# Kernel optimization log

Measured on AMD Instinct MI355X. Metric: run time of the kernel, lower is better.

Reference implementation:

```python
import jax, jax.numpy as jnp
import numpy as np

NUM_HEADS = 8
D_MODEL = 512
HEAD_DIM = D_MODEL // NUM_HEADS


def _conv1x1(x, W, b):
    # Conv1d(kernel_size=1): x [B, Cin, N], W [Cout, Cin], b [Cout] -> [B, Cout, N]
    return jnp.einsum('oi,bin->bon', W, x) + b[None, :, None]


def setup_inputs() -> dict:
    key = jax.random.key(0)
    ks = jax.random.split(key, 12)
    B, D, N, Mlen = 4, D_MODEL, 2048, 2048
    inp = {
        'query': jax.random.normal(ks[0], (B, D, N), dtype=jnp.float32),
        'key':   jax.random.normal(ks[1], (B, D, Mlen), dtype=jnp.float32),
        'value': jax.random.normal(ks[2], (B, D, Mlen), dtype=jnp.float32),
        'M':     jnp.ones((B, N, Mlen), dtype=jnp.int32),
    }
    scale = 0.02
    inp['Wq'] = jax.random.normal(ks[3], (D, D), dtype=jnp.float32) * scale
    inp['bq'] = jnp.zeros((D,), dtype=jnp.float32)
    inp['Wk'] = jax.random.normal(ks[4], (D, D), dtype=jnp.float32) * scale
    inp['bk'] = jnp.zeros((D,), dtype=jnp.float32)
    inp['Wv'] = jax.random.normal(ks[5], (D, D), dtype=jnp.float32) * scale
    inp['bv'] = jnp.zeros((D,), dtype=jnp.float32)
    inp['Wm'] = jax.random.normal(ks[6], (D, D), dtype=jnp.float32) * scale
    inp['bm'] = jnp.zeros((D,), dtype=jnp.float32)
    return inp


def reference(query, key, value, M, Wq, bq, Wk, bk, Wv, bv, Wm, bm):
    B = query.shape[0]
    # 1x1-conv projections, then channel split as [head_dim, heads] (matches torch .view)
    q = _conv1x1(query, Wq, bq).reshape(B, HEAD_DIM, NUM_HEADS, -1)  # [B, d, h, N]
    k = _conv1x1(key,   Wk, bk).reshape(B, HEAD_DIM, NUM_HEADS, -1)  # [B, d, h, M]
    v = _conv1x1(value, Wv, bv).reshape(B, HEAD_DIM, NUM_HEADS, -1)  # [B, d, h, M]
    scores = jnp.einsum('bdhn,bdhm->bhnm', q, k) / jnp.sqrt(jnp.float32(HEAD_DIM))
    # mask: positions with M==0 are disallowed -> fill with -finfo.max
    bad = (1 - M)[:, None, :, :].astype(bool)  # [B, 1, N, M], broadcasts over heads
    scores = jnp.where(bad, -jnp.finfo(scores.dtype).max, scores)
    prob = jax.nn.softmax(scores, axis=-1)  # [B, h, N, M]
    x = jnp.einsum('bhnm,bdhm->bdhn', prob, v)  # [B, d, h, N]
    out = _conv1x1(x.reshape(B, HEAD_DIM * NUM_HEADS, -1), Wm, bm)  # [B, D, N]
    return out
```

## Files before the change

### kernel.cpp

```cpp
#include <hip/hip_runtime.h>

typedef __attribute__((ext_vector_type(8))) short s8v;
typedef __attribute__((ext_vector_type(4))) float f4v;
typedef _Float16 h4 __attribute__((ext_vector_type(4)));
typedef unsigned short u16;
typedef unsigned long long u64;

#define DM 512
#define NH 8
#define HD 64
#define BB 4
#define NN 2048

__device__ __forceinline__ float bf2f(u16 x){ return __uint_as_float(((unsigned)x)<<16); }
__device__ __forceinline__ u16 f2bf(float f){
  unsigned u = __float_as_uint(f);
  u += 0x7FFFu + ((u>>16)&1u);
  return (u16)(u>>16);
}
__device__ __forceinline__ void gl2lds16(const u16* g, u16* l){
  __builtin_amdgcn_global_load_lds((__attribute__((address_space(1))) void*)(g),
                                   (__attribute__((address_space(3))) void*)(l), 16, 0, 0);
}

__global__ void k_permute(const float* Wq, const float* bq, const float* Wk, const float* bk,
                          const float* Wv, const float* bv, const float* Wm,
                          u16* Wp, u16* Wmp, float* bp){
  int blk = blockIdx.x, tid = threadIdx.x;
  if (blk < 1536){
    int t = blk >> 9, op = blk & 511;
    int srow = ((op & 63) << 3) | (op >> 6);
    const float* W = (t==0) ? Wq : ((t==1) ? Wk : Wv);
    for (int j = tid; j < 512; j += 256)
      Wp[((size_t)t*512 + op)*512 + j] = f2bf(W[(size_t)srow*512 + j]);
  } else if (blk < 2048){
    int o = blk - 1536;
    for (int c = tid; c < 512; c += 256){
      int scol = ((c & 63) << 3) | (c >> 6);
      Wmp[(size_t)o*512 + c] = f2bf(Wm[(size_t)o*512 + scol]);
    }
  } else {
    for (int idx = tid; idx < 1536; idx += 256){
      int t = idx >> 9, op = idx & 511;
      const float* bs = (t==0) ? bq : ((t==1) ? bk : bv);
      int srow = ((op & 63) << 3) | (op >> 6);
      bp[idx] = bs[srow];
    }
  }
}

__global__ __launch_bounds__(256) void k_transpose(const float* q, const float* k, const float* v, u16* XT){
  __shared__ u16 T[64*72];
  int blk = blockIdx.x, tid = threadIdx.x;
  int rt = blk & 31; blk >>= 5;
  int it = blk & 7;  blk >>= 3;
  int b  = blk & 3;  int t = blk >> 2;
  const float* src = (t==0) ? q : ((t==1) ? k : v);
  src += (size_t)b*DM*NN;
  int i0 = it*64, r0 = rt*64;
  int il = tid>>4, rj = (tid&15)*4;
  #pragma unroll
  for (int p=0;p<4;p++){
    int i = il + p*16;
    float4 vv = *(const float4*)&src[(size_t)(i0+i)*NN + r0 + rj];
    float fv[4] = {vv.x, vv.y, vv.z, vv.w};
    #pragma unroll
    for (int qq=0;qq<4;qq++){
      int r = rj + qq;
      int sr = ((r&3)<<4) | (r>>2);
      T[sr*72 + i] = f2bf(fv[qq]);
    }
  }
  __syncthreads();
  u16* dst = XT + ((size_t)(t*4+b)*NN)*DM;
  int rl = tid>>3, ib = (tid&7)*8;
  #pragma unroll
  for (int p=0;p<2;p++){
    int r = rl + p*32;
    int sr = ((r&3)<<4) | (r>>2);
    s8v vv = *(s8v*)&T[sr*72 + ib];
    *(s8v*)&dst[(size_t)(r0+r)*DM + i0 + ib] = vv;
  }
}

__global__ __launch_bounds__(256) void k_proj(const u16* XT, const u16* Wp, const float* bp,
                                              u16* P, u16* VT){
  __shared__ u16 Al[128*32];
  __shared__ u16 Bl[128*32];
  __shared__ u16 S[128*72];
  int blk = blockIdx.x, tid = threadIdx.x;
  int nt = blk & 3; int mt = blk >> 2;
  int tb = mt >> 4;
  int t  = tb >> 2, b = tb & 3;
  int r0 = (mt & 15)*128, o0 = nt*128;
  const u16* Abase = XT + ((size_t)tb*NN + r0)*DM;
  const u16* Bbase = Wp + ((size_t)t*512 + o0)*DM;

  int w = tid>>6, L = tid&63, li = L&15, lq = L>>4;
  int wr = w>>1, wc = w&1;
  int srow = tid>>2;
  int g8   = ((tid&3) ^ ((tid>>3)&3))*8;
  u16* AldsW = &Al[((tid&192))*8];
  u16* BldsW = &Bl[((tid&192))*8];
  int sw = (li>>1)&3;

  f4v acc[4][4];
  #pragma unroll
  for (int a=0;a<4;a++)
    #pragma unroll
    for (int c2=0;c2<4;c2++) acc[a][c2] = (f4v){0.f,0.f,0.f,0.f};

  for (int kk=0; kk<16; kk++){
    int k0 = kk*32;
    __syncthreads();
    #pragma unroll
    for (int c=0;c<2;c++){
      gl2lds16(&Abase[(size_t)(srow + c*64)*DM + k0 + g8], AldsW + c*2048);
      gl2lds16(&Bbase[(size_t)(srow + c*64)*DM + k0 + g8], BldsW + c*2048);
    }
    __syncthreads();
    s8v af[4], bfr[4];
    #pragma unroll
    for (int a=0;a<4;a++){
      int r = wr*64 + a*16 + li;
      af[a] = *(s8v*)&Al[r*32 + ((lq ^ sw))*8];
    }
    #pragma unroll
    for (int c2=0;c2<4;c2++){
      int r = wc*64 + c2*16 + li;
      bfr[c2] = *(s8v*)&Bl[r*32 + ((lq ^ sw))*8];
    }
    #pragma unroll
    for (int a=0;a<4;a++)
      #pragma unroll
      for (int c2=0;c2<4;c2++)
        acc[a][c2] = __builtin_amdgcn_mfma_f32_16x16x32_bf16(af[a], bfr[c2], acc[a][c2], 0, 0, 0);
  }

  if (t < 2){
    float scale = (t==0) ? 0.125f : 1.0f;
    #pragma unroll
    for (int c2=0;c2<4;c2++){
      int col = wc*64 + c2*16 + li;
      int h = (o0 + col) >> 6, d = col & 63;
      float bias = bp[t*512 + o0 + col];
      u16* Pb = P + (((size_t)tb*NH + h)*NN)*HD + d;
      #pragma unroll
      for (int a=0;a<4;a++){
        #pragma unroll
        for (int ri=0;ri<4;ri++){
          int row = r0 + wr*64 + a*16 + lq*4 + ri;
          Pb[(size_t)row*HD] = f2bf((acc[a][c2][ri] + bias)*scale);
        }
      }
    }
  } else {
    #pragma unroll
    for (int p=0;p<2;p++){
      if (wc == p){
        #pragma unroll
        for (int c2=0;c2<4;c2++){
          int cl = c2*16 + li;
          float bias = bp[2*512 + o0 + p*64 + cl];
          #pragma unroll
          for (int a=0;a<4;a++)
            #pragma unroll
            for (int ri=0;ri<4;ri++){
              _Float16 hh = (_Float16)(acc[a][c2][ri] + bias);
              S[(wr*64 + a*16 + lq*4 + ri)*72 + cl] = *(const u16*)&hh;
            }
        }
      }
      __syncthreads();
      int dl = tid & 63;
      u16* Vb = VT + (((size_t)b*NH + (o0>>6) + p)*HD + dl)*NN + r0;
      #pragma unroll
      for (int it2=0; it2<4; it2++){
        int mseg = (tid>>6) + it2*4;
        s8v vv; u16* vp = (u16*)&vv;
        #pragma unroll
        for (int j=0;j<8;j++) vp[j] = S[(mseg*8+j)*72 + dl];
        *(s8v*)&Vb[mseg*8] = vv;
      }
      __syncthreads();
    }
  }
}

__global__ void k_maskpack(const int* M, u64* bits){
  int tid = threadIdx.x;
  size_t word = (size_t)blockIdx.x*4 + (tid>>6);
  int lane = tid & 63;
  int v = M[word*64 + lane];
  u64 bal = __ballot(v == 1);
  if (lane == 0) bits[word] = bal;
}

__global__ __launch_bounds__(256) void k_maskand(const u64* bits, u64* allw){
  __shared__ u64 red[256];
  int bnt = blockIdx.x, tid = threadIdx.x;
  int mt = tid & 31, rg = tid >> 5;
  const u64* base = bits + (size_t)bnt*64*32;
  u64 v = ~0ull;
  #pragma unroll
  for (int j=0;j<8;j++) v &= base[(size_t)(rg*8+j)*32 + mt];
  red[tid] = v;
  __syncthreads();
  if (tid < 32){
    u64 a = red[tid];
    #pragma unroll
    for (int g2=1; g2<8; g2++) a &= red[g2*32 + tid];
    allw[(size_t)bnt*32 + tid] = a;
  }
}

__global__ __launch_bounds__(256) void k_flash(const u16* Pq, const u16* VT, const u64* bits,
                                               const u64* allw, u16* Xout){
  __shared__ __align__(16) char smem[19456];
  u16*   Kl  = (u16*)smem;
  u16*   Vl  = (u16*)(smem + 9216);
  float* Red = (float*)smem;
  float* lsb = (float*)(smem + 18432);

  int blk = blockIdx.x, tid = threadIdx.x;
  int nt = blk & 31; int bh = blk >> 5;
  int b = bh >> 3;
  int n0 = nt*64;
  const size_t TSZ = (size_t)BB*NH*NN*HD;
  const u16* Qb = Pq + ((size_t)bh*NN + n0)*HD;
  const u16* Kb = Pq + TSZ + (size_t)bh*NN*HD;
  const u16* Vb = VT + (size_t)bh*HD*NN;
  const u64* awp = allw + ((size_t)b*32 + nt)*32;

  int sm = tid>>3, sd = (tid&7)*8;
  int w = tid>>6, L = tid&63, li = L&15, lq = L>>4;

  s8v Qf[4][2];
  #pragma unroll
  for (int j=0;j<4;j++)
    #pragma unroll
    for (int h2=0;h2<2;h2++)
      Qf[j][h2] = *(const s8v*)&Qb[(size_t)(j*16+li)*HD + h2*32 + lq*8];

  f4v O[4][4];
  #pragma unroll
  for (int j2=0;j2<4;j2++)
    #pragma unroll
    for (int j=0;j<4;j++) O[j2][j] = (f4v){0.f,0.f,0.f,0.f};
  float ls[4] = {0.f,0.f,0.f,0.f};

  for (int mt=0; mt<32; mt++){
    int m0 = mt*64;
    u64 aw = awp[mt];
    bool fast = (aw == ~0ull);
    s8v kreg[2], vreg[2];
    #pragma unroll
    for (int p=0;p<2;p++){
      kreg[p] = *(const s8v*)&Kb[(size_t)(m0+sm+p*32)*HD + sd];
      vreg[p] = *(const s8v*)&Vb[(size_t)(sm+p*32)*NN + m0 + sd];
    }
    __syncthreads();
    #pragma unroll
    for (int p=0;p<2;p++){
      *(s8v*)&Kl[(sm+p*32)*72 + sd] = kreg[p];
      *(s8v*)&Vl[(sm+p*32)*72 + sd] = vreg[p];
    }
    __syncthreads();

    s8v Kf0 = *(s8v*)&Kl[(w*16+li)*72 + lq*8];
    s8v Kf1 = *(s8v*)&Kl[(w*16+li)*72 + 32 + lq*8];

    f4v S[4];
    #pragma unroll
    for (int j=0;j<4;j++){
      f4v c = (f4v){0.f,0.f,0.f,0.f};
      c = __builtin_amdgcn_mfma_f32_16x16x32_bf16(Kf0, Qf[j][0], c, 0, 0, 0);
      c = __builtin_amdgcn_mfma_f32_16x16x32_bf16(Kf1, Qf[j][1], c, 0, 0, 0);
      S[j] = c;
    }

    h4 Pf[4];
    if (fast){
      #pragma unroll
      for (int j=0;j<4;j++){
        float e0 = __expf(S[j][0]), e1 = __expf(S[j][1]);
        float e2 = __expf(S[j][2]), e3 = __expf(S[j][3]);
        ls[j] += (e0+e1)+(e2+e3);
        Pf[j][0] = (_Float16)e0; Pf[j][1] = (_Float16)e1;
        Pf[j][2] = (_Float16)e2; Pf[j][3] = (_Float16)e3;
      }
    } else {
      int mbit = w*16 + lq*4;
      #pragma unroll
      for (int j=0;j<4;j++){
        u64 mw = bits[((size_t)b*NN + n0 + j*16 + li)*32 + mt];
        float e[4];
        #pragma unroll
        for (int r=0;r<4;r++){
          float ev = __expf(S[j][r]);
          e[r] = ((mw>>(mbit+r)) & 1ull) ? ev : 0.f;
          Pf[j][r] = (_Float16)e[r];
        }
        ls[j] += (e[0]+e[1])+(e[2]+e[3]);
      }
    }

    #pragma unroll
    for (int j2=0;j2<4;j2++){
      h4 Vf = *(h4*)&Vl[(j2*16+li)*72 + w*16 + lq*4];
      #pragma unroll
      for (int j=0;j<4;j++)
        O[j2][j] = __builtin_amdgcn_mfma_f32_16x16x16f16(Vf, Pf[j], O[j2][j], 0, 0, 0);
    }
  }

  #pragma unroll
  for (int j=0;j<4;j++){
    float r = ls[j];
    r += __shfl_xor(r, 16); r += __shfl_xor(r, 32);
    ls[j] = r;
  }
  if (lq == 0){
    #pragma unroll
    for (int j=0;j<4;j++) lsb[w*64 + j*16 + li] = ls[j];
  }
  __syncthreads();

  #pragma unroll
  for (int ph=0; ph<4; ph++){
    if (w == ph){
      #pragma unroll
      for (int j=0;j<4;j++)
        #pragma unroll
        for (int j2=0;j2<4;j2++){
          f4v* p = (f4v*)&Red[(j*16+li)*68 + j2*16 + lq*4];
          if (ph == 0) *p = O[j2][j];
          else { f4v t = *p; t += O[j2][j]; *p = t; }
        }
    }
    __syncthreads();
  }

  int n = tid>>2, d0 = (tid&3)*16;
  float s = lsb[n] + lsb[64+n] + lsb[128+n] + lsb[192+n];
  float inv = (s > 0.f) ? 1.0f/s : 0.f;
  int h = bh & 7;
  u16* Xo = Xout + ((size_t)b*NN + n0 + n)*DM + h*HD + d0;
  u16 tmp[16];
  #pragma unroll
  for (int e2=0;e2<4;e2++){
    f4v vv = *(f4v*)&Red[n*68 + d0 + e2*4];
    #pragma unroll
    for (int q2=0;q2<4;q2++) tmp[e2*4+q2] = f2bf(vv[q2]*inv);
  }
  *(s8v*)&Xo[0] = *(s8v*)&tmp[0];
  *(s8v*)&Xo[8] = *(s8v*)&tmp[8];
}

__global__ __launch_bounds__(256) void k_out(const u16* Wmp, const u16* Xout, const float* bm, float* out){
  __shared__ u16 Al[128*32];
  __shared__ u16 Bl[128*32];
  int blk = blockIdx.x, tid = threadIdx.x;
  int nt = blk & 15; blk >>= 4;
  int ot = blk & 3;  int b = blk >> 2;
  int o0 = ot*128, n0 = nt*128;
  const u16* Abase = Wmp + (size_t)o0*DM;
  const u16* Bbase = Xout + ((size_t)b*NN + n0)*DM;

  int w = tid>>6, L = tid&63, li = L&15, lq = L>>4;
  int wr = w>>1, wc = w&1;
  int srow = tid>>2;
  int g8   = ((tid&3) ^ ((tid>>3)&3))*8;
  u16* AldsW = &Al[((tid&192))*8];
  u16* BldsW = &Bl[((tid&192))*8];
  int sw = (li>>1)&3;

  f4v acc[4][4];
  #pragma unroll
  for (int a=0;a<4;a++)
    #pragma unroll
    for (int c2=0;c2<4;c2++) acc[a][c2] = (f4v){0.f,0.f,0.f,0.f};

  for (int kk=0; kk<16; kk++){
    int k0 = kk*32;
    __syncthreads();
    #pragma unroll
    for (int c=0;c<2;c++){
      gl2lds16(&Abase[(size_t)(srow + c*64)*DM + k0 + g8], AldsW + c*2048);
      gl2lds16(&Bbase[(size_t)(srow + c*64)*DM + k0 + g8], BldsW + c*2048);
    }
    __syncthreads();
    s8v af[4], bfr[4];
    #pragma unroll
    for (int a=0;a<4;a++){
      int r = wr*64 + a*16 + li;
      af[a] = *(s8v*)&Al[r*32 + ((lq ^ sw))*8];
    }
    #pragma unroll
    for (int c2=0;c2<4;c2++){
      int r = wc*64 + c2*16 + li;
      bfr[c2] = *(s8v*)&Bl[r*32 + ((lq ^ sw))*8];
    }
    #pragma unroll
    for (int a=0;a<4;a++)
      #pragma unroll
      for (int c2=0;c2<4;c2++)
        acc[a][c2] = __builtin_amdgcn_mfma_f32_16x16x32_bf16(af[a], bfr[c2], acc[a][c2], 0, 0, 0);
  }

  #pragma unroll
  for (int a=0;a<4;a++){
    #pragma unroll
    for (int ri=0;ri<4;ri++){
      int o = o0 + wr*64 + a*16 + lq*4 + ri;
      float bias = bm[o];
      float* ob = out + ((size_t)b*DM + o)*NN + n0 + wc*64;
      #pragma unroll
      for (int c2=0;c2<4;c2++)
        ob[c2*16 + li] = acc[a][c2][ri] + bias;
    }
  }
}

extern "C" void kernel_launch(void* const* d_in, const int* in_sizes, int n_in,
                              void* d_out, int out_size, void* d_ws, size_t ws_size,
                              hipStream_t stream){
  const float* q  = (const float*)d_in[0];
  const float* k  = (const float*)d_in[1];
  const float* v  = (const float*)d_in[2];
  const int*   M  = (const int*)d_in[3];
  const float* Wq = (const float*)d_in[4];
  const float* bq = (const float*)d_in[5];
  const float* Wk = (const float*)d_in[6];
  const float* bk = (const float*)d_in[7];
  const float* Wv = (const float*)d_in[8];
  const float* bv = (const float*)d_in[9];
  const float* Wm = (const float*)d_in[10];
  const float* bm = (const float*)d_in[11];

  char* ws = (char*)d_ws;
  u16*   XT   = (u16*)(ws + 0);
  u16*   P    = (u16*)(ws + 25165824);
  u16*   VT   = (u16*)(ws + 41943040);
  u16*   Wp   = (u16*)(ws + 50331648);
  u16*   Wmp  = (u16*)(ws + 51904512);
  float* bp   = (float*)(ws + 52428800);
  u64*   bits = (u64*)(ws + 52434944);
  u16*   Xout = (u16*)(ws + 54532096);
  u64*   allw = (u64*)(ws + 62920704);
  float* out  = (float*)d_out;

  k_permute<<<2049, 256, 0, stream>>>(Wq, bq, Wk, bk, Wv, bv, Wm, Wp, Wmp, bp);
  k_transpose<<<3072, 256, 0, stream>>>(q, k, v, XT);
  k_proj<<<768, 256, 0, stream>>>(XT, Wp, bp, P, VT);
  k_maskpack<<<65536, 256, 0, stream>>>(M, bits);
  k_maskand<<<128, 256, 0, stream>>>(bits, allw);
  k_flash<<<1024, 256, 0, stream>>>(P, VT, bits, allw, Xout);
  k_out<<<256, 256, 0, stream>>>(Wmp, Xout, bm, out);
}
```

Before: 299.2 us.

## Stage Q/K projection stores via LDS, load K/V directly in flash, halve k_out tile

The Q/K projection epilogue now stages bf16 results in shared memory and writes them out as coalesced 16-byte rows, replacing the strided per-element stores. The flash kernel drops the LDS staging and the two barriers per tile, loading K and V fragments straight from global memory into registers. The output GEMM uses a 64-row output tile with twice as many blocks, for better occupancy and GPU fill. The trade-off is that flash now makes uncoalesced or duplicated global loads and relies on cache hits, and k_out reloads the B tile more often.

```diff
diff --git a/kernel.cpp b/kernel.cpp
--- a/kernel.cpp
+++ b/kernel.cpp
@@ -140,19 +140,29 @@
   if (t < 2){
     float scale = (t==0) ? 0.125f : 1.0f;
     #pragma unroll
-    for (int c2=0;c2<4;c2++){
-      int col = wc*64 + c2*16 + li;
-      int h = (o0 + col) >> 6, d = col & 63;
-      float bias = bp[t*512 + o0 + col];
-      u16* Pb = P + (((size_t)tb*NH + h)*NN)*HD + d;
-      #pragma unroll
-      for (int a=0;a<4;a++){
+    for (int p=0;p<2;p++){
+      if (wc == p){
         #pragma unroll
-        for (int ri=0;ri<4;ri++){
-          int row = r0 + wr*64 + a*16 + lq*4 + ri;
-          Pb[(size_t)row*HD] = f2bf((acc[a][c2][ri] + bias)*scale);
+        for (int c2=0;c2<4;c2++){
+          int cl = c2*16 + li;
+          float bias = bp[t*512 + o0 + p*64 + cl];
+          #pragma unroll
+          for (int a=0;a<4;a++)
+            #pragma unroll
+            for (int ri=0;ri<4;ri++)
+              S[(wr*64 + a*16 + lq*4 + ri)*72 + cl] = f2bf((acc[a][c2][ri] + bias)*scale);
         }
       }
+      __syncthreads();
+      int row = tid>>1, cb = (tid&1)*32;
+      int hh = (o0>>6) + p;
+      u16* Pb = P + (((size_t)tb*NH + hh)*NN + r0 + row)*HD + cb;
+      #pragma unroll
+      for (int c=0;c<4;c++){
+        s8v vv = *(s8v*)&S[row*72 + cb + c*8];
+        *(s8v*)&Pb[c*8] = vv;
+      }
+      __syncthreads();
     }
   } else {
     #pragma unroll
@@ -216,9 +226,7 @@
 
 __global__ __launch_bounds__(256) void k_flash(const u16* Pq, const u16* VT, const u64* bits,
                                                const u64* allw, u16* Xout){
-  __shared__ __align__(16) char smem[19456];
-  u16*   Kl  = (u16*)smem;
-  u16*   Vl  = (u16*)(smem + 9216);
+  __shared__ __align__(16) char smem[18432 + 1024];
   float* Red = (float*)smem;
   float* lsb = (float*)(smem + 18432);
 
@@ -232,7 +240,6 @@
   const u16* Vb = VT + (size_t)bh*HD*NN;
   const u64* awp = allw + ((size_t)b*32 + nt)*32;
 
-  int sm = tid>>3, sd = (tid&7)*8;
   int w = tid>>6, L = tid&63, li = L&15, lq = L>>4;
 
   s8v Qf[4][2];
@@ -248,27 +255,21 @@
     #pragma unroll
     for (int j=0;j<4;j++) O[j2][j] = (f4v){0.f,0.f,0.f,0.f};
   float ls[4] = {0.f,0.f,0.f,0.f};
+
+  const u16* Krow = Kb + (size_t)(w*16 + li)*HD + lq*8;
+  const u16* Vrow = Vb + (size_t)li*NN + w*16 + lq*4;
 
   for (int mt=0; mt<32; mt++){
     int m0 = mt*64;
     u64 aw = awp[mt];
     bool fast = (aw == ~0ull);
-    s8v kreg[2], vreg[2];
-    #pragma unroll
-    for (int p=0;p<2;p++){
-      kreg[p] = *(const s8v*)&Kb[(size_t)(m0+sm+p*32)*HD + sd];
-      vreg[p] = *(const s8v*)&Vb[(size_t)(sm+p*32)*NN + m0 + sd];
-    }
-    __syncthreads();
-    #pragma unroll
-    for (int p=0;p<2;p++){
-      *(s8v*)&Kl[(sm+p*32)*72 + sd] = kreg[p];
-      *(s8v*)&Vl[(sm+p*32)*72 + sd] = vreg[p];
-    }
-    __syncthreads();
-
-    s8v Kf0 = *(s8v*)&Kl[(w*16+li)*72 + lq*8];
-    s8v Kf1 = *(s8v*)&Kl[(w*16+li)*72 + 32 + lq*8];
+
+    s8v Kf0 = *(const s8v*)&Krow[(size_t)m0*HD];
+    s8v Kf1 = *(const s8v*)&Krow[(size_t)m0*HD + 32];
+    h4 Vf[4];
+    #pragma unroll
+    for (int j2=0;j2<4;j2++)
+      Vf[j2] = *(const h4*)&Vrow[(size_t)(j2*16)*NN + m0];
 
     f4v S[4];
     #pragma unroll
@@ -306,12 +307,10 @@
     }
 
     #pragma unroll
-    for (int j2=0;j2<4;j2++){
-      h4 Vf = *(h4*)&Vl[(j2*16+li)*72 + w*16 + lq*4];
+    for (int j2=0;j2<4;j2++)
       #pragma unroll
       for (int j=0;j<4;j++)
-        O[j2][j] = __builtin_amdgcn_mfma_f32_16x16x16f16(Vf, Pf[j], O[j2][j], 0, 0, 0);
-    }
+        O[j2][j] = __builtin_amdgcn_mfma_f32_16x16x16f16(Vf[j2], Pf[j], O[j2][j], 0, 0, 0);
   }
 
   #pragma unroll
@@ -358,63 +357,62 @@
 }
 
 __global__ __launch_bounds__(256) void k_out(const u16* Wmp, const u16* Xout, const float* bm, float* out){
-  __shared__ u16 Al[128*32];
+  __shared__ u16 Al[64*32];
   __shared__ u16 Bl[128*32];
   int blk = blockIdx.x, tid = threadIdx.x;
   int nt = blk & 15; blk >>= 4;
-  int ot = blk & 3;  int b = blk >> 2;
-  int o0 = ot*128, n0 = nt*128;
+  int ot = blk & 7;  int b = blk >> 3;
+  int o0 = ot*64, n0 = nt*128;
   const u16* Abase = Wmp + (size_t)o0*DM;
   const u16* Bbase = Xout + ((size_t)b*NN + n0)*DM;
 
   int w = tid>>6, L = tid&63, li = L&15, lq = L>>4;
-  int wr = w>>1, wc = w&1;
+  int wo = w&1, wn = w>>1;
   int srow = tid>>2;
   int g8   = ((tid&3) ^ ((tid>>3)&3))*8;
   u16* AldsW = &Al[((tid&192))*8];
   u16* BldsW = &Bl[((tid&192))*8];
   int sw = (li>>1)&3;
 
-  f4v acc[4][4];
-  #pragma unroll
-  for (int a=0;a<4;a++)
+  f4v acc[2][4];
+  #pragma unroll
+  for (int a=0;a<2;a++)
     #pragma unroll
     for (int c2=0;c2<4;c2++) acc[a][c2] = (f4v){0.f,0.f,0.f,0.f};
 
   for (int kk=0; kk<16; kk++){
     int k0 = kk*32;
     __syncthreads();
-    #pragma unroll
-    for (int c=0;c<2;c++){
-      gl2lds16(&Abase[(size_t)(srow + c*64)*DM + k0 + g8], AldsW + c*2048);
+    gl2lds16(&Abase[(size_t)srow*DM + k0 + g8], AldsW);
+    #pragma unroll
+    for (int c=0;c<2;c++)
       gl2lds16(&Bbase[(size_t)(srow + c*64)*DM + k0 + g8], BldsW + c*2048);
-    }
     __syncthreads();
-    s8v af[4], bfr[4];
-    #pragma unroll
-    for (int a=0;a<4;a++){
-      int r = wr*64 + a*16 + li;
+    s8v af[2], bfr[4];
+    #pragma unroll
+    for (int a=0;a<2;a++){
+      int r = wo*32 + a*16 + li;
       af[a] = *(s8v*)&Al[r*32 + ((lq ^ sw))*8];
     }
     #pragma unroll
     for (int c2=0;c2<4;c2++){
-      int r = wc*64 + c2*16 + li;
+      int r = wn*64 + c2*16 + li;
       bfr[c2] = *(s8v*)&Bl[r*32 + ((lq ^ sw))*8];
     }
     #pragma unroll
-    for (int a=0;a<4;a++)
+    for (int a=0;a<2;a++)
       #pragma unroll
       for (int c2=0;c2<4;c2++)
         acc[a][c2] = __builtin_amdgcn_mfma_f32_16x16x32_bf16(af[a], bfr[c2], acc[a][c2], 0, 0, 0);
   }
 
   #pragma unroll
-  for (int a=0;a<4;a++){
+  for (int a=0;a<2;a++){
     #pragma unroll
     for (int ri=0;ri<4;ri++){
-      int o = o0 + wr*64 + a*16 + lq*4 + ri;
+      int o = o0 + wo*32 + a*16 + lq*4 + ri;
       float bias = bm[o];
-      float* ob = out + ((size_t)b*DM + o)*NN + n0 + wc*64;
+      float* ob = out + ((size_t)b*DM + o)*NN + n0 + wn*64;
       #pragma unroll
       for (int c2=0;c2<4;c2++)
         ob[c2*16 + li] = acc[a][c2][ri] + bias;
@@ -456,5 +454,5 @@
   k_maskpack<<<65536, 256, 0, stream>>>(M, bits);
   k_maskand<<<128, 256, 0, stream>>>(bits, allw);
   k_flash<<<1024, 256, 0, stream>>>(P, VT, bits, allw, Xout);
-  k_out<<<256, 256, 0, stream>>>(Wmp, Xout, bm, out);
-}
+  k_out<<<512, 256, 0, stream>>>(Wmp, Xout, bm, out);
+}
```

Result: slower. 325.8 us (+8.9%).
